# Kernel optimization log

Hardware: AMD Instinct MI355X
Metric: run time of the kernel (lower is better)

The kernel has to match this reference:

```python
import jax, jax.numpy as jnp
import numpy as np
import math

# Model config (matches init_kwargs)
V, D, H, L, DFF, S_MAX = 32000, 512, 8, 6, 2048, 1024
DK = D // H


def _layernorm(x, g, b, eps=1e-5):
    m = jnp.mean(x, axis=-1, keepdims=True)
    v = jnp.mean(jnp.square(x - m), axis=-1, keepdims=True)
    return (x - m) / jnp.sqrt(v + eps) * g + b


def _pos_encoding(seq_len, d_model):
    # sin on even dims, cos on odd dims
    pos = jnp.arange(seq_len, dtype=jnp.float32)[:, None]          # [S,1]
    div = jnp.exp(jnp.arange(0, d_model, 2, dtype=jnp.float32) *
                  (-math.log(10000.0) / d_model))                   # [D/2]
    ang = pos * div                                                 # [S,D/2]
    pe = jnp.stack([jnp.sin(ang), jnp.cos(ang)], axis=-1)           # [S,D/2,2]
    return pe.reshape(seq_len, d_model)                             # [S,D]


def setup_inputs() -> dict:
    key = jax.random.key(0)
    ks = jax.random.split(key, 24)
    sd = 0.02

    def n(k, shape):
        return jax.random.normal(k, shape, jnp.float32) * sd

    B, S = 2, 1024
    return {
        "tokens": jax.random.randint(ks[0], (B, S), 0, V, dtype=jnp.int32),
        "tok_emb": n(ks[1], (V, D)),
        # attention projections, [L, D, D] stored as (in, out)
        "Wq": n(ks[2], (L, D, D)), "bq": jnp.zeros((L, D)),
        "Wk": n(ks[3], (L, D, D)), "bk": jnp.zeros((L, D)),
        "Wv": n(ks[4], (L, D, D)), "bv": jnp.zeros((L, D)),
        "Wo": n(ks[5], (L, D, D)), "bo": jnp.zeros((L, D)),
        "ln1_g": jnp.ones((L, D)), "ln1_b": jnp.zeros((L, D)),
        "W1": n(ks[6], (L, D, DFF)), "b1": jnp.zeros((L, DFF)),
        "W2": n(ks[7], (L, DFF, D)), "b2": jnp.zeros((L, D)),
        "ln2_g": jnp.ones((L, D)), "ln2_b": jnp.zeros((L, D)),
        "lnf_g": jnp.ones((D,)), "lnf_b": jnp.zeros((D,)),
        "Wout": n(ks[8], (D, V)), "bout": jnp.zeros((V,)),
    }


def reference(tokens, tok_emb, Wq, bq, Wk, bk, Wv, bv, Wo, bo,
              ln1_g, ln1_b, W1, b1, W2, b2, ln2_g, ln2_b,
              lnf_g, lnf_b, Wout, bout):
    B, S = tokens.shape
    x = tok_emb[tokens] * math.sqrt(D) + _pos_encoding(S, D)[None]   # [B,S,D]
    causal = jnp.tril(jnp.ones((S, S), dtype=bool))[None, None]       # [1,1,S,S]
    scale = math.sqrt(DK)

    attns = []
    for l in range(L):
        q = (x @ Wq[l] + bq[l]).reshape(B, S, H, DK).transpose(0, 2, 1, 3)
        k = (x @ Wk[l] + bk[l]).reshape(B, S, H, DK).transpose(0, 2, 1, 3)
        v = (x @ Wv[l] + bv[l]).reshape(B, S, H, DK).transpose(0, 2, 1, 3)
        scores = jnp.einsum('bhsk,bhtk->bhst', q, k) / scale           # [B,H,S,S]
        scores = jnp.where(causal, scores, -1e9)
        a = jax.nn.softmax(scores, axis=-1)
        ctx = jnp.einsum('bhst,bhtk->bhsk', a, v)                      # [B,H,S,DK]
        ctx = ctx.transpose(0, 2, 1, 3).reshape(B, S, D)
        attn_out = ctx @ Wo[l] + bo[l]
        x = _layernorm(x + attn_out, ln1_g[l], ln1_b[l])
        h = jax.nn.gelu(x @ W1[l] + b1[l], approximate=False)          # torch GELU (exact)
        ff = h @ W2[l] + b2[l]
        x = _layernorm(x + ff, ln2_g[l], ln2_b[l])
        attns.append(a)

    x = _layernorm(x, lnf_g, lnf_b)
    logits = x @ Wout + bout                                           # [B,S,V]
    return logits, jnp.stack(attns)                                    # attn: [L,B,H,S,S]
```

## Files before the change

### kernel.cpp

```cpp
#include <hip/hip_runtime.h>
#include <math.h>

#define NB 2
#define NS 1024
#define NH 8
#define NDK 64
#define ND 512
#define NDFF 2048
#define NV 32000
#define NL 6
#define MROWS (NB * NS)
#define QKVLD (3 * ND)

using bf16_t = __bf16;
using bf16x4 = __attribute__((ext_vector_type(4))) __bf16;
using bf16x8 = __attribute__((ext_vector_type(8))) __bf16;
using f32x4  = __attribute__((ext_vector_type(4))) float;

__device__ __forceinline__ void gload_lds16(const bf16_t* g, bf16_t* l) {
  __builtin_amdgcn_global_load_lds(
      (const __attribute__((address_space(1))) void*)g,
      (__attribute__((address_space(3))) void*)l, 16, 0, 0);
}

__device__ __forceinline__ float gelu_exact(float v) {
  return 0.5f * v * (1.0f + erff(v * 0.7071067811865476f));
}

__global__ __launch_bounds__(256)
void prep_kernel(const int* __restrict__ tokens, const float* __restrict__ emb,
                 const float* __restrict__ Wq, const float* __restrict__ Wk,
                 const float* __restrict__ Wv, const float* __restrict__ Wo,
                 const float* __restrict__ W1, const float* __restrict__ W2,
                 const float* __restrict__ Wout,
                 bf16_t* __restrict__ WqkvT, bf16_t* __restrict__ WoT,
                 bf16_t* __restrict__ W1T, bf16_t* __restrict__ W2T,
                 bf16_t* __restrict__ WoutT,
                 float* __restrict__ x, bf16_t* __restrict__ xb) {
  __shared__ bf16_t T[64][72];
  const int id = blockIdx.x;
  const int tid = threadIdx.x;

  if (id >= 8608) {
    const int row = id - 8608;
    const int s = row & (NS - 1);
    const int tok = tokens[row];
    const float SQRTD = 22.627416997969522f;
    const float C = -9.210340371976184f / (float)ND;
#pragma unroll
    for (int i = 0; i < 2; ++i) {
      const int d = tid + i * 256;
      const int pair = d >> 1;
      const float div = expf((float)(2 * pair) * C);
      const float ang = (float)s * div;
      const float pe = (d & 1) ? cosf(ang) : sinf(ang);
      const float v = emb[(size_t)tok * ND + d] * SQRTD + pe;
      x[(size_t)row * ND + d] = v;
      xb[(size_t)row * ND + d] = (bf16_t)v;
    }
    return;
  }

  const float* src; bf16_t* dst; int K, N, n0, k0;
  if (id < 1536) {
    const int z = id >> 6, t = id & 63;
    const int mat = z / 6, layer = z % 6;
    src = ((mat == 0) ? Wq : (mat == 1) ? Wk : (mat == 2) ? Wv : Wo) + (size_t)layer * ND * ND;
    dst = (mat < 3) ? (WqkvT + (size_t)layer * QKVLD * ND + (size_t)mat * ND * ND)
                    : (WoT + (size_t)layer * ND * ND);
    K = ND; N = ND; n0 = (t & 7) * 64; k0 = (t >> 3) * 64;
  } else if (id < 3072) {
    const int idx = id - 1536, layer = idx >> 8, t = idx & 255;
    src = W1 + (size_t)layer * ND * NDFF; dst = W1T + (size_t)layer * NDFF * ND;
    K = ND; N = NDFF; n0 = (t & 31) * 64; k0 = (t >> 5) * 64;
  } else if (id < 4608) {
    const int idx = id - 3072, layer = idx >> 8, t = idx & 255;
    src = W2 + (size_t)layer * NDFF * ND; dst = W2T + (size_t)layer * ND * NDFF;
    K = NDFF; N = ND; n0 = (t & 7) * 64; k0 = (t >> 3) * 64;
  } else {
    const int t = id - 4608;
    src = Wout; dst = WoutT;
    K = ND; N = NV; n0 = (t % 500) * 64; k0 = (t / 500) * 64;
  }

#pragma unroll
  for (int it = 0; it < 4; ++it) {
    const int k = (tid >> 4) + it * 16;
    const int c = (tid & 15) * 4;
    const float4 v = *(const float4*)&src[(size_t)(k0 + k) * N + n0 + c];
    T[c + 0][k] = (bf16_t)v.x;
    T[c + 1][k] = (bf16_t)v.y;
    T[c + 2][k] = (bf16_t)v.z;
    T[c + 3][k] = (bf16_t)v.w;
  }
  __syncthreads();
  const int n = tid >> 2, kk = (tid & 3) * 16;
  bf16x8 a = *(const bf16x8*)&T[n][kk];
  bf16x8 b2v = *(const bf16x8*)&T[n][kk + 8];
  *(bf16x8*)&dst[(size_t)(n0 + n) * K + k0 + kk] = a;
  *(bf16x8*)&dst[(size_t)(n0 + n) * K + k0 + kk + 8] = b2v;
}

__global__ __launch_bounds__(256)
void add_ln_kernel(float* __restrict__ x, const float* __restrict__ y,
                   const float* __restrict__ g, const float* __restrict__ bb,
                   bf16_t* __restrict__ xb) {
  const int row = blockIdx.x, tid = threadIdx.x;
  const size_t base = (size_t)row * ND;
  float v0 = x[base + tid], v1 = x[base + tid + 256];
  if (y) { v0 += y[base + tid]; v1 += y[base + tid + 256]; }
  __shared__ float red[256];
  red[tid] = v0 + v1; __syncthreads();
  for (int o = 128; o > 0; o >>= 1) {
    if (tid < o) red[tid] += red[tid + o];
    __syncthreads();
  }
  const float mean = red[0] * (1.f / (float)ND);
  __syncthreads();
  const float d0 = v0 - mean, d1 = v1 - mean;
  red[tid] = d0 * d0 + d1 * d1; __syncthreads();
  for (int o = 128; o > 0; o >>= 1) {
    if (tid < o) red[tid] += red[tid + o];
    __syncthreads();
  }
  const float inv = 1.f / sqrtf(red[0] * (1.f / (float)ND) + 1e-5f);
  const float o0 = d0 * inv * g[tid]       + bb[tid];
  const float o1 = d1 * inv * g[tid + 256] + bb[tid + 256];
  x[base + tid] = o0;
  x[base + tid + 256] = o1;
  xb[base + tid] = (bf16_t)o0; xb[base + tid + 256] = (bf16_t)o1;
}

template <int ACT, int OUTBF>
__global__ __launch_bounds__(256)
void gemm_bt(const bf16_t* __restrict__ A, const bf16_t* __restrict__ Wt,
             const float* __restrict__ B0,
             void* __restrict__ Cout, int N, int K, int lda, int ldc) {
  __shared__ bf16_t As[128 * 64];
  __shared__ bf16_t Bs[128 * 64];
  const int tid = threadIdx.x, lane = tid & 63, w = tid >> 6;
  const int wm = w >> 1, wn = w & 1;
  const int lcol = lane & 15, hi = lane >> 4;

  const int nwg = gridDim.x * gridDim.y;
  const int flat = blockIdx.y * gridDim.x + blockIdx.x;
  const int q = nwg >> 3, r = nwg & 7;
  const int xcd = flat & 7, idx = flat >> 3;
  const int nf = (xcd < r ? xcd * (q + 1) : r * (q + 1) + (xcd - r) * q) + idx;
  const int m0 = (nf % gridDim.x) * 128, n0 = (nf / gridDim.x) * 128;

  const int sr8 = lane >> 3;
  const int sslot = lane & 7;

  f32x4 acc[4][4] = {};

  for (int k0 = 0; k0 < K; k0 += 64) {
#pragma unroll
    for (int t = 0; t < 2; ++t) {
#pragma unroll
      for (int c = 0; c < 2; ++c) {
        const int rbase = t * 64 + w * 16 + c * 8;
        const int row = rbase + sr8;
        const int ks = sslot ^ (row & 7);
        gload_lds16(&A[(size_t)(m0 + row) * lda + k0 + ks * 8], &As[rbase * 64]);
        gload_lds16(&Wt[(size_t)(n0 + row) * K + k0 + ks * 8], &Bs[rbase * 64]);
      }
    }
    __syncthreads();

#pragma unroll
    for (int kk = 0; kk < 2; ++kk) {
      bf16x8 af[4], bf[4];
#pragma unroll
      for (int m = 0; m < 4; ++m) {
        const int rr = wm * 64 + m * 16 + lcol;
        af[m] = *(const bf16x8*)&As[rr * 64 + (((kk * 4 + hi) ^ (rr & 7)) * 8)];
      }
#pragma unroll
      for (int n = 0; n < 4; ++n) {
        const int rr = wn * 64 + n * 16 + lcol;
        bf[n] = *(const bf16x8*)&Bs[rr * 64 + (((kk * 4 + hi) ^ (rr & 7)) * 8)];
      }
#pragma unroll
      for (int m = 0; m < 4; ++m)
#pragma unroll
        for (int n = 0; n < 4; ++n)
          acc[m][n] = __builtin_amdgcn_mfma_f32_16x16x32_bf16(bf[n], af[m], acc[m][n], 0, 0, 0);
    }
    __syncthreads();
  }

#pragma unroll
  for (int m = 0; m < 4; ++m) {
    const int row = m0 + wm * 64 + m * 16 + lcol;
#pragma unroll
    for (int n = 0; n < 4; ++n) {
      const int col = n0 + wn * 64 + n * 16 + hi * 4;
      const f32x4 bv = *(const f32x4*)&B0[col];
      f32x4 v;
#pragma unroll
      for (int i = 0; i < 4; ++i) {
        float t = acc[m][n][i] + bv[i];
        if (ACT == 1) t = gelu_exact(t);
        v[i] = t;
      }
      if (OUTBF) {
        bf16x4 o;
#pragma unroll
        for (int i = 0; i < 4; ++i) o[i] = (bf16_t)v[i];
        *(bf16x4*)&((bf16_t*)Cout)[(size_t)row * ldc + col] = o;
      } else {
        __builtin_nontemporal_store(v, (f32x4*)&((float*)Cout)[(size_t)row * ldc + col]);
      }
    }
  }
}

__global__ __launch_bounds__(256)
void gemm_qkv64(const bf16_t* __restrict__ A, const bf16_t* __restrict__ Wt,
                const float* __restrict__ B0, const float* __restrict__ B1,
                const float* __restrict__ B2,
                bf16_t* __restrict__ Cout, int K, int lda, int ldc) {
  __shared__ bf16_t As[64 * 128];
  __shared__ bf16_t Bs[64 * 128];
  const int tid = threadIdx.x, lane = tid & 63, w = tid >> 6;
  const int wm = w >> 1, wn = w & 1;
  const int lcol = lane & 15, hi = lane >> 4;
  const int m0 = blockIdx.x * 64, n0 = blockIdx.y * 64;
  const int sr4 = lane >> 4, sslot = lane & 15;

  f32x4 acc[2][2] = {};

  for (int k0 = 0; k0 < K; k0 += 128) {
#pragma unroll
    for (int c = 0; c < 4; ++c) {
      const int rbase = w * 16 + c * 4;
      const int row = rbase + sr4;
      const int ks = sslot ^ (row & 15);
      gload_lds16(&A[(size_t)(m0 + row) * lda + k0 + ks * 8], &As[rbase * 128]);
      gload_lds16(&Wt[(size_t)(n0 + row) * K + k0 + ks * 8], &Bs[rbase * 128]);
    }
    __syncthreads();

#pragma unroll
    for (int kk = 0; kk < 4; ++kk) {
      bf16x8 af[2], bf[2];
#pragma unroll
      for (int m = 0; m < 2; ++m) {
        const int rr = wm * 32 + m * 16 + lcol;
        af[m] = *(const bf16x8*)&As[rr * 128 + (((kk * 4 + hi) ^ (rr & 15)) * 8)];
      }
#pragma unroll
      for (int n = 0; n < 2; ++n) {
        const int rr = wn * 32 + n * 16 + lcol;
        bf[n] = *(const bf16x8*)&Bs[rr * 128 + (((kk * 4 + hi) ^ (rr & 15)) * 8)];
      }
#pragma unroll
      for (int m = 0; m < 2; ++m)
#pragma unroll
        for (int n = 0; n < 2; ++n)
          acc[m][n] = __builtin_amdgcn_mfma_f32_16x16x32_bf16(bf[n], af[m], acc[m][n], 0, 0, 0);
    }
    __syncthreads();
  }

#pragma unroll
  for (int m = 0; m < 2; ++m) {
    const int row = m0 + wm * 32 + m * 16 + lcol;
#pragma unroll
    for (int n = 0; n < 2; ++n) {
      const int col = n0 + wn * 32 + n * 16 + hi * 4;
      const int sel = col >> 9;
      const float* Bp = (sel == 0) ? B0 : (sel == 1) ? B1 : B2;
      const f32x4 bv = *(const f32x4*)&Bp[col & 511];
      bf16x4 o;
#pragma unroll
      for (int i = 0; i < 4; ++i) o[i] = (bf16_t)(acc[m][n][i] + bv[i]);
      *(bf16x4*)&Cout[(size_t)row * ldc + col] = o;
    }
  }
}

template <int ACT>
__global__ __launch_bounds__(256)
void gemm_bt64(const bf16_t* __restrict__ A, const bf16_t* __restrict__ Wt,
               const float* __restrict__ bias,
               float* __restrict__ Cout, int K, int lda, int ldc) {
  __shared__ bf16_t As[64 * 128];
  __shared__ bf16_t Bs[64 * 128];
  const int tid = threadIdx.x, lane = tid & 63, w = tid >> 6;
  const int wm = w >> 1, wn = w & 1;
  const int lcol = lane & 15, hi = lane >> 4;
  const int m0 = blockIdx.x * 64, n0 = blockIdx.y * 64;
  const int sr4 = lane >> 4, sslot = lane & 15;

  f32x4 acc[2][2] = {};

  for (int k0 = 0; k0 < K; k0 += 128) {
#pragma unroll
    for (int c = 0; c < 4; ++c) {
      const int rbase = w * 16 + c * 4;
      const int row = rbase + sr4;
      const int ks = sslot ^ (row & 15);
      gload_lds16(&A[(size_t)(m0 + row) * lda + k0 + ks * 8], &As[rbase * 128]);
      gload_lds16(&Wt[(size_t)(n0 + row) * K + k0 + ks * 8], &Bs[rbase * 128]);
    }
    __syncthreads();

#pragma unroll
    for (int kk = 0; kk < 4; ++kk) {
      bf16x8 af[2], bf[2];
#pragma unroll
      for (int m = 0; m < 2; ++m) {
        const int rr = wm * 32 + m * 16 + lcol;
        af[m] = *(const bf16x8*)&As[rr * 128 + (((kk * 4 + hi) ^ (rr & 15)) * 8)];
      }
#pragma unroll
      for (int n = 0; n < 2; ++n) {
        const int rr = wn * 32 + n * 16 + lcol;
        bf[n] = *(const bf16x8*)&Bs[rr * 128 + (((kk * 4 + hi) ^ (rr & 15)) * 8)];
      }
#pragma unroll
      for (int m = 0; m < 2; ++m)
#pragma unroll
        for (int n = 0; n < 2; ++n)
          acc[m][n] = __builtin_amdgcn_mfma_f32_16x16x32_bf16(bf[n], af[m], acc[m][n], 0, 0, 0);
    }
    __syncthreads();
  }

#pragma unroll
  for (int m = 0; m < 2; ++m) {
    const int row = m0 + wm * 32 + m * 16 + lcol;
#pragma unroll
    for (int n = 0; n < 2; ++n) {
      const int col = n0 + wn * 32 + n * 16 + hi * 4;
      const f32x4 bv = *(const f32x4*)&bias[col];
      f32x4 v;
#pragma unroll
      for (int i = 0; i < 4; ++i) {
        float t = acc[m][n][i] + bv[i];
        if (ACT == 1) t = gelu_exact(t);
        v[i] = t;
      }
      *(f32x4*)&Cout[(size_t)row * ldc + col] = v;
    }
  }
}

__global__ __launch_bounds__(256)
void attn_fused(const bf16_t* __restrict__ qkv, float* __restrict__ probs,
                bf16_t* __restrict__ ctx) {
  const int qt = 15 - blockIdx.x;
  const int h = blockIdx.y, b = blockIdx.z;
  const int q0 = qt * 64;
  const int NTT = (q0 >> 7) + 1;
  const int qmax = q0 + 63;
  const int tid = threadIdx.x, lane = tid & 63, wq = tid >> 6;
  const int lcol = lane & 15, hi = lane >> 4;

  __shared__ bf16_t Qs[64][72];
  __shared__ bf16_t Ks[128][72];
  __shared__ bf16_t Vs[64][132];
  __shared__ bf16_t Ps[64][132];

  {
    const int r = tid >> 2, c = (tid & 3) * 16;
    const bf16_t* src = &qkv[((size_t)(b * NS + q0 + r)) * QKVLD + h * NDK + c];
    *(bf16x8*)&Qs[r][c]     = *(const bf16x8*)&src[0];
    *(bf16x8*)&Qs[r][c + 8] = *(const bf16x8*)&src[8];
  }
  __syncthreads();
  const bf16x8 qf0 = *(const bf16x8*)&Qs[wq * 16 + lcol][hi * 8];
  const bf16x8 qf1 = *(const bf16x8*)&Qs[wq * 16 + lcol][32 + hi * 8];
  const int qrow = q0 + wq * 16 + lcol;
  const float scale = 0.125f;

  float m_run = -1e30f, s_run = 0.f;

  for (int tt = 0; tt < NTT; ++tt) {
    const int t0 = tt * 128;
    const int fmax = min(8, ((qmax - t0) >> 4) + 1);
    {
      const int r = tid >> 1, cb = (tid & 1) * 32;
      const bf16_t* src = &qkv[((size_t)(b * NS + t0 + r)) * QKVLD + ND + h * NDK + cb];
#pragma unroll
      for (int j = 0; j < 4; ++j)
        *(bf16x8*)&Ks[r][cb + j * 8] = *(const bf16x8*)&src[j * 8];
    }
    __syncthreads();

    float tmax = -1e30f;
    f32x4 sc[8];
#pragma unroll
    for (int f = 0; f < 8; ++f) {
      if (f >= fmax) break;
      f32x4 s4 = {};
      const bf16x8 ka0 = *(const bf16x8*)&Ks[f * 16 + lcol][hi * 8];
      const bf16x8 ka1 = *(const bf16x8*)&Ks[f * 16 + lcol][32 + hi * 8];
      s4 = __builtin_amdgcn_mfma_f32_16x16x32_bf16(ka0, qf0, s4, 0, 0, 0);
      s4 = __builtin_amdgcn_mfma_f32_16x16x32_bf16(ka1, qf1, s4, 0, 0, 0);
#pragma unroll
      for (int i = 0; i < 4; ++i) {
        const int t = t0 + f * 16 + hi * 4 + i;
        const float v = (t <= qrow) ? s4[i] * scale : -1e30f;
        s4[i] = v;
        tmax = fmaxf(tmax, v);
      }
      sc[f] = s4;
    }
    tmax = fmaxf(tmax, __shfl_xor(tmax, 16));
    tmax = fmaxf(tmax, __shfl_xor(tmax, 32));
    const float m_new = fmaxf(m_run, tmax);
    float sum = 0.f;
#pragma unroll
    for (int f = 0; f < 8; ++f) {
      if (f >= fmax) break;
#pragma unroll
      for (int i = 0; i < 4; ++i) sum += __expf(sc[f][i] - m_new);
    }
    sum += __shfl_xor(sum, 16);
    sum += __shfl_xor(sum, 32);
    s_run = s_run * __expf(m_run - m_new) + sum;
    m_run = m_new;
    __syncthreads();
  }
  const float inv = 1.f / s_run;

  f32x4 cacc[4] = {};
  const size_t prow = (((size_t)b * NH + h) * NS + qrow) * NS;
  for (int tt = NTT - 1; tt >= 0; --tt) {
    const int t0 = tt * 128;
    const int fmax = min(8, ((qmax - t0) >> 4) + 1);
    if (tt != NTT - 1) {
      const int r = tid >> 1, cb = (tid & 1) * 32;
      const bf16_t* src = &qkv[((size_t)(b * NS + t0 + r)) * QKVLD + ND + h * NDK + cb];
#pragma unroll
      for (int j = 0; j < 4; ++j)
        *(bf16x8*)&Ks[r][cb + j * 8] = *(const bf16x8*)&src[j * 8];
    }
    {
#pragma unroll
      for (int it = 0; it < 2; ++it) {
        const int t4 = (tid >> 4) * 4 + it * 64;
        const int dk4 = (tid & 15) * 4;
        bf16x4 rr[4];
#pragma unroll
        for (int i = 0; i < 4; ++i)
          rr[i] = *(const bf16x4*)&qkv[((size_t)(b * NS + t0 + t4 + i)) * QKVLD + 2 * ND + h * NDK + dk4];
#pragma unroll
        for (int j = 0; j < 4; ++j) {
          bf16x4 c;
#pragma unroll
          for (int i = 0; i < 4; ++i) c[i] = rr[i][j];
          *(bf16x4*)&Vs[dk4 + j][t4] = c;
        }
      }
    }
    __syncthreads();

    const f32x4 zf = {0.f, 0.f, 0.f, 0.f};
    const bf16x4 zb = {(bf16_t)0.f, (bf16_t)0.f, (bf16_t)0.f, (bf16_t)0.f};
#pragma unroll
    for (int f = 0; f < 8; ++f) {
      if (f < fmax) {
        f32x4 s4 = {};
        const bf16x8 ka0 = *(const bf16x8*)&Ks[f * 16 + lcol][hi * 8];
        const bf16x8 ka1 = *(const bf16x8*)&Ks[f * 16 + lcol][32 + hi * 8];
        s4 = __builtin_amdgcn_mfma_f32_16x16x32_bf16(ka0, qf0, s4, 0, 0, 0);
        s4 = __builtin_amdgcn_mfma_f32_16x16x32_bf16(ka1, qf1, s4, 0, 0, 0);
        f32x4 pw;
        bf16x4 pb;
#pragma unroll
        for (int i = 0; i < 4; ++i) {
          const int t = t0 + f * 16 + hi * 4 + i;
          const float v = (t <= qrow) ? s4[i] * scale : -1e30f;
          const float p = __expf(v - m_run) * inv;
          pw[i] = p;
          pb[i] = (bf16_t)p;
        }
        __builtin_nontemporal_store(pw, (f32x4*)&probs[prow + t0 + f * 16 + hi * 4]);
        *(bf16x4*)&Ps[wq * 16 + lcol][f * 16 + hi * 4] = pb;
      } else {
        __builtin_nontemporal_store(zf, (f32x4*)&probs[prow + t0 + f * 16 + hi * 4]);
        *(bf16x4*)&Ps[wq * 16 + lcol][f * 16 + hi * 4] = zb;
      }
    }

#pragma unroll
    for (int ks = 0; ks < 4; ++ks) {
      const bf16x8 pf = *(const bf16x8*)&Ps[wq * 16 + lcol][ks * 32 + hi * 8];
#pragma unroll
      for (int df = 0; df < 4; ++df) {
        const bf16x8 vf = *(const bf16x8*)&Vs[df * 16 + lcol][ks * 32 + hi * 8];
        cacc[df] = __builtin_amdgcn_mfma_f32_16x16x32_bf16(vf, pf, cacc[df], 0, 0, 0);
      }
    }
    __syncthreads();
  }

#pragma unroll
  for (int df = 0; df < 4; ++df) {
    bf16x4 o;
#pragma unroll
    for (int i = 0; i < 4; ++i) o[i] = (bf16_t)cacc[df][i];
    *(bf16x4*)&ctx[((size_t)(b * NS + q0 + wq * 16 + lcol)) * ND + h * NDK + df * 16 + hi * 4] = o;
  }

  const int z0 = NTT * 128;
  const int nz = (NS - z0) >> 2;
  if (nz > 0) {
    const f32x4 zf = {0.f, 0.f, 0.f, 0.f};
    for (int idx = tid; idx < 64 * nz; idx += 256) {
      const int r = idx / nz, c = (idx - r * nz) * 4;
      __builtin_nontemporal_store(zf,
          (f32x4*)&probs[(((size_t)b * NH + h) * NS + q0 + r) * NS + z0 + c]);
    }
  }
}

extern "C" void kernel_launch(void* const* d_in, const int* in_sizes, int n_in,
                              void* d_out, int out_size, void* d_ws, size_t ws_size,
                              hipStream_t stream) {
  const int*   tokens  = (const int*)d_in[0];
  const float* tok_emb = (const float*)d_in[1];
  const float* Wq = (const float*)d_in[2];
  const float* bq = (const float*)d_in[3];
  const float* Wk = (const float*)d_in[4];
  const float* bk = (const float*)d_in[5];
  const float* Wv = (const float*)d_in[6];
  const float* bv = (const float*)d_in[7];
  const float* Wo = (const float*)d_in[8];
  const float* bo = (const float*)d_in[9];
  const float* ln1_g = (const float*)d_in[10];
  const float* ln1_b = (const float*)d_in[11];
  const float* W1 = (const float*)d_in[12];
  const float* b1 = (const float*)d_in[13];
  const float* W2 = (const float*)d_in[14];
  const float* b2 = (const float*)d_in[15];
  const float* ln2_g = (const float*)d_in[16];
  const float* ln2_b = (const float*)d_in[17];
  const float* lnf_g = (const float*)d_in[18];
  const float* lnf_b = (const float*)d_in[19];
  const float* Wout = (const float*)d_in[20];
  const float* bout = (const float*)d_in[21];

  float* logits   = (float*)d_out;
  float* attn_all = (float*)d_out + (size_t)NB * NS * NV;

  char* w = (char*)d_ws;
  float* x    = (float*)w;  w += (size_t)4 << 20;
  float* tmp  = (float*)w;  w += (size_t)4 << 20;
  bf16_t* xb  = (bf16_t*)w; w += (size_t)2 << 20;
  bf16_t* qkv = (bf16_t*)w; w += (size_t)6 << 20;
  bf16_t* ctx = (bf16_t*)w; w += (size_t)2 << 20;
  bf16_t* hh  = (bf16_t*)w; w += (size_t)8 << 20;
  bf16_t* WqkvT = (bf16_t*)w; w += (size_t)6 * QKVLD * ND * 2;
  bf16_t* WoT   = (bf16_t*)w; w += (size_t)6 * ND * ND * 2;
  bf16_t* W1T   = (bf16_t*)w; w += (size_t)6 * NDFF * ND * 2;
  bf16_t* W2T   = (bf16_t*)w; w += (size_t)6 * ND * NDFF * 2;
  bf16_t* WoutT = (bf16_t*)w; w += (size_t)NV * ND * 2;
  if ((size_t)(w - (char*)d_ws) > ws_size) return;

  const int M = MROWS;

  prep_kernel<<<10656, 256, 0, stream>>>(tokens, tok_emb, Wq, Wk, Wv, Wo, W1, W2, Wout,
                                         WqkvT, WoT, W1T, W2T, WoutT, x, xb);

  const dim3 gQKV(M / 64, QKVLD / 64);
  const dim3 gFF1(M / 128, NDFF / 128);
  const dim3 gOut(M / 128, NV / 128);
  const dim3 g64(M / 64, ND / 64);
  const dim3 gAttn(16, NH, NB);

  for (int l = 0; l < NL; ++l) {
    gemm_qkv64<<<gQKV, 256, 0, stream>>>(xb, WqkvT + (size_t)l * QKVLD * ND,
        bq + l * ND, bk + l * ND, bv + l * ND, qkv, ND, ND, QKVLD);

    float* probs_l = attn_all + (size_t)l * NB * NH * NS * NS;
    attn_fused<<<gAttn, 256, 0, stream>>>(qkv, probs_l, ctx);

    gemm_bt64<0><<<g64, 256, 0, stream>>>(ctx, WoT + (size_t)l * ND * ND,
        bo + l * ND, tmp, ND, ND, ND);
    add_ln_kernel<<<M, 256, 0, stream>>>(x, tmp, ln1_g + l * ND, ln1_b + l * ND, xb);

    gemm_bt<1, 1><<<gFF1, 256, 0, stream>>>(xb, W1T + (size_t)l * NDFF * ND,
        b1 + l * NDFF, hh, NDFF, ND, ND, NDFF);
    gemm_bt64<0><<<g64, 256, 0, stream>>>(hh, W2T + (size_t)l * ND * NDFF,
        b2 + l * ND, tmp, NDFF, NDFF, ND);
    add_ln_kernel<<<M, 256, 0, stream>>>(x, tmp, ln2_g + l * ND, ln2_b + l * ND, xb);
  }

  add_ln_kernel<<<M, 256, 0, stream>>>(x, nullptr, lnf_g, lnf_b, xb);

  gemm_bt<0, 0><<<gOut, 256, 0, stream>>>(xb, WoutT, bout,
      logits, NV, ND, ND, NV);
}
```

Baseline: 747.8 us.

## Split-K the Wo and W2 GEMMs and retile FF1 onto the 64x64 GEMM

```diff
diff --git a/kernel.cpp b/kernel.cpp
--- a/kernel.cpp
+++ b/kernel.cpp
@@ -102,13 +102,15 @@
 }
 
 __global__ __launch_bounds__(256)
-void add_ln_kernel(float* __restrict__ x, const float* __restrict__ y,
+void add_ln_kernel(float* __restrict__ x, const float* __restrict__ y0,
+                   const float* __restrict__ y1,
                    const float* __restrict__ g, const float* __restrict__ bb,
                    bf16_t* __restrict__ xb) {
   const int row = blockIdx.x, tid = threadIdx.x;
   const size_t base = (size_t)row * ND;
   float v0 = x[base + tid], v1 = x[base + tid + 256];
-  if (y) { v0 += y[base + tid]; v1 += y[base + tid + 256]; }
+  if (y0) { v0 += y0[base + tid]; v1 += y0[base + tid + 256]; }
+  if (y1) { v0 += y1[base + tid]; v1 += y1[base + tid + 256]; }
   __shared__ float red[256];
   red[tid] = v0 + v1; __syncthreads();
   for (int o = 128; o > 0; o >>= 1) {
@@ -281,11 +283,11 @@
   }
 }
 
-template <int ACT>
+template <int ACT, int OUTBF>
 __global__ __launch_bounds__(256)
-void gemm_bt64(const bf16_t* __restrict__ A, const bf16_t* __restrict__ Wt,
-               const float* __restrict__ bias,
-               float* __restrict__ Cout, int K, int lda, int ldc) {
+void gemm64(const bf16_t* __restrict__ A, const bf16_t* __restrict__ Wt,
+            const float* __restrict__ bias,
+            void* __restrict__ Cout, int K, int lda, int ldc, size_t zstride) {
   __shared__ bf16_t As[64 * 128];
   __shared__ bf16_t Bs[64 * 128];
   const int tid = threadIdx.x, lane = tid & 63, w = tid >> 6;
@@ -293,10 +295,12 @@
   const int lcol = lane & 15, hi = lane >> 4;
   const int m0 = blockIdx.x * 64, n0 = blockIdx.y * 64;
   const int sr4 = lane >> 4, sslot = lane & 15;
+  const int kc = K / gridDim.z;
+  const int kbeg = blockIdx.z * kc;
 
   f32x4 acc[2][2] = {};
 
-  for (int k0 = 0; k0 < K; k0 += 128) {
+  for (int k0 = kbeg; k0 < kbeg + kc; k0 += 128) {
 #pragma unroll
     for (int c = 0; c < 4; ++c) {
       const int rbase = w * 16 + c * 4;
@@ -335,7 +339,8 @@
 #pragma unroll
     for (int n = 0; n < 2; ++n) {
       const int col = n0 + wn * 32 + n * 16 + hi * 4;
-      const f32x4 bv = *(const f32x4*)&bias[col];
+      f32x4 bv = {0.f, 0.f, 0.f, 0.f};
+      if (blockIdx.z == 0) bv = *(const f32x4*)&bias[col];
       f32x4 v;
 #pragma unroll
       for (int i = 0; i < 4; ++i) {
@@ -343,7 +348,14 @@
         if (ACT == 1) t = gelu_exact(t);
         v[i] = t;
       }
-      *(f32x4*)&Cout[(size_t)row * ldc + col] = v;
+      if (OUTBF) {
+        bf16x4 o;
+#pragma unroll
+        for (int i = 0; i < 4; ++i) o[i] = (bf16_t)v[i];
+        *(bf16x4*)&((bf16_t*)Cout)[(size_t)row * ldc + col] = o;
+      } else {
+        *(f32x4*)&((float*)Cout)[blockIdx.z * zstride + (size_t)row * ldc + col] = v;
+      }
     }
   }
 }
@@ -550,7 +562,7 @@
 
   char* w = (char*)d_ws;
   float* x    = (float*)w;  w += (size_t)4 << 20;
-  float* tmp  = (float*)w;  w += (size_t)4 << 20;
+  float* tmp  = (float*)w;  w += (size_t)8 << 20;
   bf16_t* xb  = (bf16_t*)w; w += (size_t)2 << 20;
   bf16_t* qkv = (bf16_t*)w; w += (size_t)6 << 20;
   bf16_t* ctx = (bf16_t*)w; w += (size_t)2 << 20;
@@ -563,14 +575,16 @@
   if ((size_t)(w - (char*)d_ws) > ws_size) return;
 
   const int M = MROWS;
+  const size_t U = (size_t)M * ND;
+  float* tmp1 = tmp + U;
 
   prep_kernel<<<10656, 256, 0, stream>>>(tokens, tok_emb, Wq, Wk, Wv, Wo, W1, W2, Wout,
                                          WqkvT, WoT, W1T, W2T, WoutT, x, xb);
 
   const dim3 gQKV(M / 64, QKVLD / 64);
-  const dim3 gFF1(M / 128, NDFF / 128);
+  const dim3 gFF1(M / 64, NDFF / 64);
   const dim3 gOut(M / 128, NV / 128);
-  const dim3 g64(M / 64, ND / 64);
+  const dim3 g64s(M / 64, ND / 64, 2);
   const dim3 gAttn(16, NH, NB);
 
   for (int l = 0; l < NL; ++l) {
@@ -580,18 +594,18 @@
     float* probs_l = attn_all + (size_t)l * NB * NH * NS * NS;
     attn_fused<<<gAttn, 256, 0, stream>>>(qkv, probs_l, ctx);
 
-    gemm_bt64<0><<<g64, 256, 0, stream>>>(ctx, WoT + (size_t)l * ND * ND,
-        bo + l * ND, tmp, ND, ND, ND);
-    add_ln_kernel<<<M, 256, 0, stream>>>(x, tmp, ln1_g + l * ND, ln1_b + l * ND, xb);
-
-    gemm_bt<1, 1><<<gFF1, 256, 0, stream>>>(xb, W1T + (size_t)l * NDFF * ND,
-        b1 + l * NDFF, hh, NDFF, ND, ND, NDFF);
-    gemm_bt64<0><<<g64, 256, 0, stream>>>(hh, W2T + (size_t)l * ND * NDFF,
-        b2 + l * ND, tmp, NDFF, NDFF, ND);
-    add_ln_kernel<<<M, 256, 0, stream>>>(x, tmp, ln2_g + l * ND, ln2_b + l * ND, xb);
-  }
-
-  add_ln_kernel<<<M, 256, 0, stream>>>(x, nullptr, lnf_g, lnf_b, xb);
+    gemm64<0, 0><<<g64s, 256, 0, stream>>>(ctx, WoT + (size_t)l * ND * ND,
+        bo + l * ND, tmp, ND, ND, ND, U);
+    add_ln_kernel<<<M, 256, 0, stream>>>(x, tmp, tmp1, ln1_g + l * ND, ln1_b + l * ND, xb);
+
+    gemm64<1, 1><<<gFF1, 256, 0, stream>>>(xb, W1T + (size_t)l * NDFF * ND,
+        b1 + l * NDFF, hh, ND, ND, NDFF, 0);
+    gemm64<0, 0><<<g64s, 256, 0, stream>>>(hh, W2T + (size_t)l * ND * NDFF,
+        b2 + l * ND, tmp, NDFF, NDFF, ND, U);
+    add_ln_kernel<<<M, 256, 0, stream>>>(x, tmp, tmp1, ln2_g + l * ND, ln2_b + l * ND, xb);
+  }
+
+  add_ln_kernel<<<M, 256, 0, stream>>>(x, nullptr, nullptr, lnf_g, lnf_b, xb);
 
   gemm_bt<0, 0><<<gOut, 256, 0, stream>>>(xb, WoutT, bout,
       logits, NV, ND, ND, NV);
```

Result: faster. 684.6 us (-8.5%).
